# Kernel tuning notes

Hardware: AMD Instinct MI355X
Metric: run time of the kernel (lower is better)

## Reference

```python
import jax, jax.numpy as jnp
import numpy as np

# Precompute flat gather indices replicating matA's banded structure.
# Row (layer l, offset i) of matA sums d[i : i+l], for l in 1..255, i in 0..255-l.
# Equivalently diff = cumsum_pad[i+l] - cumsum_pad[i].
def _build_indices():
    lo, hi, lid = [], [], []
    for l in range(1, 256):
        n = 256 - l
        i = np.arange(n)
        lo.append(i)
        hi.append(i + l)
        lid.append(np.full(n, l - 1))
    return (np.concatenate(lo), np.concatenate(hi), np.concatenate(lid))

_IDX_LO, _IDX_HI, _LAYER_ID = _build_indices()  # each length 32640
IDX_LO = jnp.asarray(_IDX_LO)
IDX_HI = jnp.asarray(_IDX_HI)
LAYER_ID = jnp.asarray(_LAYER_ID)
# elements averaged per layer: B * (256 - l)
_COUNTS = (256 - np.arange(1, 256)).astype(np.float32)
COUNTS = jnp.asarray(_COUNTS)


def setup_inputs() -> dict:
    key = jax.random.key(0)
    k1, k2, k3 = jax.random.split(key, 3)
    B = 512
    d1layer = jax.random.normal(k1, (B, 1, 255), dtype=jnp.float32)
    hvec = jax.random.normal(k2, (B, 32640), dtype=jnp.float32)
    mask = jax.random.uniform(k3, (B, 255), dtype=jnp.float32)
    return {"d1layer": d1layer, "hvec": hvec, "mask": mask}


def reference(d1layer, hvec, mask):
    B = d1layer.shape[0]
    m = jnp.power(mask, 2.5)  # [B, 255]
    d = d1layer[:, 0, :]  # [B, 255]
    # padded cumulative sum: c[:, k] = sum_{j<k} d[:, j], shape [B, 256]
    c = jnp.concatenate(
        [jnp.zeros((B, 1), dtype=d.dtype), jnp.cumsum(d, axis=1)], axis=1
    )
    # banded windowed sums for all 32640 (layer, offset) pairs at once
    matAd = c[:, IDX_HI] - c[:, IDX_LO]  # [B, 32640]
    w = m[:, LAYER_ID]  # [B, 32640], mask[:, layer-1] broadcast over offsets
    sq = jnp.square(matAd - hvec) * w  # [B, 32640]
    per_layer_sum = jax.ops.segment_sum(
        jnp.sum(sq, axis=0), LAYER_ID, num_segments=255
    )  # [255]
    loss_layers = per_layer_sum / (COUNTS * jnp.float32(B))  # per-layer mean
    return jnp.mean(loss_layers)
```

## Files before the change

kernel.cpp:

```cpp
#include <hip/hip_runtime.h>

#define NLAYER 255
#define SEQ    256
#define TOTJ   32640
#define CHUNKS 8
#define CHUNK_J (TOTJ / CHUNKS)
#define CHUNK_F4 (CHUNK_J / 4)
#define THREADS 256

__global__ void build_table(unsigned short* __restrict__ table) {
    int l = blockIdx.x + 1;
    int n = 256 - l;
    int i = threadIdx.x;
    if (i < n) {
        int base = 256 * (l - 1) - ((l - 1) * l) / 2;
        table[base + i] = (unsigned short)((l - 1) | (i << 8));
    }
}

__global__ __launch_bounds__(THREADS) void main_kernel(
        const float* __restrict__ d1layer,
        const float* __restrict__ hvec,
        const float* __restrict__ mask,
        const unsigned short* __restrict__ table,
        float* __restrict__ partials)
{
    __shared__ float c[SEQ];
    __shared__ float w[NLAYER];
    __shared__ float red[THREADS / 64];

    const int b     = blockIdx.y;
    const int chunk = blockIdx.x;
    const int t     = threadIdx.x;

    c[t] = (t > 0) ? d1layer[b * NLAYER + (t - 1)] : 0.0f;
    if (t < NLAYER) {
        float mk = mask[b * NLAYER + t];
        w[t] = mk * mk * sqrtf(mk) / (float)(NLAYER - t);
    }
    __syncthreads();

    #pragma unroll
    for (int off = 1; off < SEQ; off <<= 1) {
        float v   = c[t];
        float add = (t >= off) ? c[t - off] : 0.0f;
        __syncthreads();
        c[t] = v + add;
        __syncthreads();
    }

    const float4* hv4 =
        (const float4*)(hvec + (size_t)b * TOTJ + (size_t)chunk * CHUNK_J);
    const unsigned short* tb = table + chunk * CHUNK_J;

    float acc = 0.0f;
    for (int f4 = t; f4 < CHUNK_F4; f4 += THREADS) {
        float4 h = hv4[f4];
        ushort4 tv = *(const ushort4*)(tb + f4 * 4);

        int l0 = tv.x & 0xFF, lo0 = tv.x >> 8;
        int l1 = tv.y & 0xFF, lo1 = tv.y >> 8;
        int l2 = tv.z & 0xFF, lo2 = tv.z >> 8;
        int l3 = tv.w & 0xFF, lo3 = tv.w >> 8;

        float d0 = (c[lo0 + l0 + 1] - c[lo0]) - h.x;
        float d1 = (c[lo1 + l1 + 1] - c[lo1]) - h.y;
        float d2 = (c[lo2 + l2 + 1] - c[lo2]) - h.z;
        float d3 = (c[lo3 + l3 + 1] - c[lo3]) - h.w;

        acc += d0 * d0 * w[l0];
        acc += d1 * d1 * w[l1];
        acc += d2 * d2 * w[l2];
        acc += d3 * d3 * w[l3];
    }

    #pragma unroll
    for (int off = 32; off > 0; off >>= 1)
        acc += __shfl_down(acc, off, 64);
    int lane = t & 63, wid = t >> 6;
    if (lane == 0) red[wid] = acc;
    __syncthreads();
    if (t == 0) {
        float s = 0.0f;
        #pragma unroll
        for (int i = 0; i < THREADS / 64; ++i) s += red[i];
        partials[b * gridDim.x + chunk] = s;
    }
}

__global__ void reduce_kernel(const float* __restrict__ partials, int n, int B,
                              float* __restrict__ out) {
    __shared__ float red[16];
    float acc = 0.0f;
    for (int i = threadIdx.x; i < n; i += blockDim.x) acc += partials[i];
    #pragma unroll
    for (int off = 32; off > 0; off >>= 1)
        acc += __shfl_down(acc, off, 64);
    int lane = threadIdx.x & 63, wid = threadIdx.x >> 6;
    if (lane == 0) red[wid] = acc;
    __syncthreads();
    if (threadIdx.x == 0) {
        float s = 0.0f;
        int nw = blockDim.x >> 6;
        for (int i = 0; i < nw; ++i) s += red[i];
        out[0] = s / ((float)NLAYER * (float)B);
    }
}

extern "C" void kernel_launch(void* const* d_in, const int* in_sizes, int n_in,
                              void* d_out, int out_size, void* d_ws, size_t ws_size,
                              hipStream_t stream) {
    const float* d1layer = (const float*)d_in[0];
    const float* hvec    = (const float*)d_in[1];
    const float* mask    = (const float*)d_in[2];
    float* out = (float*)d_out;

    const int B = in_sizes[2] / NLAYER;

    unsigned short* table = (unsigned short*)d_ws;
    float* partials = (float*)((char*)d_ws + TOTJ * sizeof(unsigned short));

    build_table<<<NLAYER, 256, 0, stream>>>(table);

    dim3 grid(CHUNKS, B);
    main_kernel<<<grid, THREADS, 0, stream>>>(d1layer, hvec, mask, table, partials);

    reduce_kernel<<<1, 1024, 0, stream>>>(partials, CHUNKS * B, B, out);
}
```

Before: 104.3 us.

## Replace index table with paired-layer indexing and wave-shuffle prefix scan

Removes the precomputed (layer, offset) lookup table and its build kernel. Each block instead processes pairs of complementary layers (p and 256-p), which together have exactly 255 elements, so thread t maps to an element arithmetically. The shared-memory Hillis-Steele prefix sum is replaced with a wave-level shuffle scan plus per-wave offsets, which needs fewer barriers. The grid shrinks from 8 to 4 blocks per batch row and loads change from float4 to scalar per thread, which may reduce memory-level parallelism.

```diff
diff --git a/kernel.cpp b/kernel.cpp
--- a/kernel.cpp
+++ b/kernel.cpp
@@ -3,96 +3,91 @@
 #define NLAYER 255
 #define SEQ    256
 #define TOTJ   32640
-#define CHUNKS 8
-#define CHUNK_J (TOTJ / CHUNKS)
-#define CHUNK_F4 (CHUNK_J / 4)
+#define PG     4
+#define PASSES_PER_GROUP 32
 #define THREADS 256
-
-__global__ void build_table(unsigned short* __restrict__ table) {
-    int l = blockIdx.x + 1;
-    int n = 256 - l;
-    int i = threadIdx.x;
-    if (i < n) {
-        int base = 256 * (l - 1) - ((l - 1) * l) / 2;
-        table[base + i] = (unsigned short)((l - 1) | (i << 8));
-    }
-}
 
 __global__ __launch_bounds__(THREADS) void main_kernel(
         const float* __restrict__ d1layer,
         const float* __restrict__ hvec,
         const float* __restrict__ mask,
-        const unsigned short* __restrict__ table,
         float* __restrict__ partials)
 {
     __shared__ float c[SEQ];
-    __shared__ float w[NLAYER];
+    __shared__ float w[SEQ];
+    __shared__ float wsum[THREADS / 64];
     __shared__ float red[THREADS / 64];
 
-    const int b     = blockIdx.y;
-    const int chunk = blockIdx.x;
-    const int t     = threadIdx.x;
+    const int g = blockIdx.x;
+    const int b = blockIdx.y;
+    const int t = threadIdx.x;
+    const int lane = t & 63;
+    const int wid  = t >> 6;
 
-    c[t] = (t > 0) ? d1layer[b * NLAYER + (t - 1)] : 0.0f;
     if (t < NLAYER) {
         float mk = mask[b * NLAYER + t];
-        w[t] = mk * mk * sqrtf(mk) / (float)(NLAYER - t);
+        w[t + 1] = mk * mk * sqrtf(mk) / (float)(NLAYER - t);
     }
+
+    float v = (t > 0) ? d1layer[b * NLAYER + (t - 1)] : 0.0f;
+    #pragma unroll
+    for (int off = 1; off < 64; off <<= 1) {
+        float u = __shfl_up(v, off, 64);
+        if (lane >= off) v += u;
+    }
+    if (lane == 63) wsum[wid] = v;
+    __syncthreads();
+    float woff = 0.0f;
+    #pragma unroll
+    for (int i = 0; i < THREADS / 64; ++i)
+        if (i < wid) woff += wsum[i];
+    c[t] = v + woff;
     __syncthreads();
 
-    #pragma unroll
-    for (int off = 1; off < SEQ; off <<= 1) {
-        float v   = c[t];
-        float add = (t >= off) ? c[t - off] : 0.0f;
-        __syncthreads();
-        c[t] = v + add;
-        __syncthreads();
-    }
-
-    const float4* hv4 =
-        (const float4*)(hvec + (size_t)b * TOTJ + (size_t)chunk * CHUNK_J);
-    const unsigned short* tb = table + chunk * CHUNK_J;
+    const float* hrow = hvec + (size_t)b * TOTJ;
+    const int p0 = g * PASSES_PER_GROUP + 1;
 
     float acc = 0.0f;
-    for (int f4 = t; f4 < CHUNK_F4; f4 += THREADS) {
-        float4 h = hv4[f4];
-        ushort4 tv = *(const ushort4*)(tb + f4 * 4);
+    #pragma unroll 4
+    for (int pp = 0; pp < PASSES_PER_GROUP; ++pp) {
+        const int p  = p0 + pp;
+        const int n  = 256 - p;
+        const int m1 = p - 1;
+        const int S1 = 256 * m1 - ((m1 * (m1 + 1)) >> 1);
+        const int m2 = 256 - p;
+        const int S2 = 256 * m2 - ((m2 * (m2 + 1)) >> 1);
 
-        int l0 = tv.x & 0xFF, lo0 = tv.x >> 8;
-        int l1 = tv.y & 0xFF, lo1 = tv.y >> 8;
-        int l2 = tv.z & 0xFF, lo2 = tv.z >> 8;
-        int l3 = tv.w & 0xFF, lo3 = tv.w >> 8;
-
-        float d0 = (c[lo0 + l0 + 1] - c[lo0]) - h.x;
-        float d1 = (c[lo1 + l1 + 1] - c[lo1]) - h.y;
-        float d2 = (c[lo2 + l2 + 1] - c[lo2]) - h.z;
-        float d3 = (c[lo3 + l3 + 1] - c[lo3]) - h.w;
-
-        acc += d0 * d0 * w[l0];
-        acc += d1 * d1 * w[l1];
-        acc += d2 * d2 * w[l2];
-        acc += d3 * d3 * w[l3];
+        if (t < NLAYER) {
+            const bool first = t < n;
+            const int layer = first ? p : (257 - p);
+            const int i     = first ? t : (t - n);
+            const int hidx  = first ? (S1 + t) : (S2 + t - n);
+            float h  = hrow[hidx];
+            float dd = (c[i + layer] - c[i]) - h;
+            acc += dd * dd * w[layer];
+        }
     }
 
     #pragma unroll
     for (int off = 32; off > 0; off >>= 1)
         acc += __shfl_down(acc, off, 64);
-    int lane = t & 63, wid = t >> 6;
     if (lane == 0) red[wid] = acc;
     __syncthreads();
     if (t == 0) {
         float s = 0.0f;
         #pragma unroll
         for (int i = 0; i < THREADS / 64; ++i) s += red[i];
-        partials[b * gridDim.x + chunk] = s;
+        partials[b * PG + g] = s;
     }
 }
 
-__global__ void reduce_kernel(const float* __restrict__ partials, int n, int B,
-                              float* __restrict__ out) {
-    __shared__ float red[16];
+__global__ __launch_bounds__(256) void reduce_kernel(
+        const float* __restrict__ partials, int n, int B,
+        float* __restrict__ out)
+{
+    __shared__ float red[4];
     float acc = 0.0f;
-    for (int i = threadIdx.x; i < n; i += blockDim.x) acc += partials[i];
+    for (int i = threadIdx.x; i < n; i += 256) acc += partials[i];
     #pragma unroll
     for (int off = 32; off > 0; off >>= 1)
         acc += __shfl_down(acc, off, 64);
@@ -101,8 +96,8 @@
     __syncthreads();
     if (threadIdx.x == 0) {
         float s = 0.0f;
-        int nw = blockDim.x >> 6;
-        for (int i = 0; i < nw; ++i) s += red[i];
+        #pragma unroll
+        for (int i = 0; i < 4; ++i) s += red[i];
         out[0] = s / ((float)NLAYER * (float)B);
     }
 }
@@ -117,13 +112,9 @@
 
     const int B = in_sizes[2] / NLAYER;
 
-    unsigned short* table = (unsigned short*)d_ws;
-    float* partials = (float*)((char*)d_ws + TOTJ * sizeof(unsigned short));
+    float* partials = (float*)d_ws;
 
-    build_table<<<NLAYER, 256, 0, stream>>>(table);
-
-    dim3 grid(CHUNKS, B);
-    main_kernel<<<grid, THREADS, 0, stream>>>(d1layer, hvec, mask, table, partials);
-
-    reduce_kernel<<<1, 1024, 0, stream>>>(partials, CHUNKS * B, B, out);
+    dim3 grid(PG, B);
+    main_kernel<<<grid, THREADS, 0, stream>>>(d1layer, hvec, mask, partials);
+    reduce_kernel<<<1, 256, 0, stream>>>(partials, PG * B, B, out);
 }
```

Result: slower. 112.2 us (+7.6%).
